# Performance work log

Hardware: AMD Instinct MI355X
Metric: run time of the kernel (lower is better)

## Reference

```python
import jax, jax.numpy as jnp
import numpy as np

B, T, S = 8, 96, 192          # batch, tgt_len (decoder steps), src_len (encoder memory)
D_IN, D_MEM = 512, 512        # input_size (query dim), mem_size (memory dim)


def setup_inputs() -> dict:
    key = jax.random.key(0)
    ks = jax.random.split(key, 9)
    w = 0.02  # init scale for learned params
    inputs = jax.random.normal(ks[0], (B, T, D_IN), jnp.float32)
    mems = jax.random.normal(ks[1], (B, S, D_MEM), jnp.float32)
    # lengths in [1, S] so no row is fully masked
    mem_masks = jax.random.randint(ks[2], (B,), 1, S + 1)
    Wq = jax.random.normal(ks[3], (D_MEM, D_IN), jnp.float32) * w    # linear_q.weight (no bias)
    Wc = jax.random.normal(ks[4], (D_MEM, D_MEM), jnp.float32) * w   # linear_c.weight
    bc = jax.random.normal(ks[5], (D_MEM,), jnp.float32) * w         # linear_c.bias
    v = jax.random.normal(ks[6], (D_MEM,), jnp.float32) * w          # v.weight (mem_size -> 1)
    Wout = jax.random.normal(ks[7], (D_IN, D_MEM + D_IN), jnp.float32) * w  # linear_out.weight
    bout = jax.random.normal(ks[8], (D_IN,), jnp.float32) * w        # linear_out.bias
    return dict(inputs=inputs, mems=mems, mem_masks=mem_masks,
                Wq=Wq, Wc=Wc, bc=bc, v=v, Wout=Wout, bout=bout)


def reference(inputs, mems, mem_masks, Wq, Wc, bc, v, Wout, bout):
    # score(): additive (tanh-MLP) attention
    wq = jnp.einsum('btd,md->btm', inputs, Wq)          # [B,T,Dm]
    uh = jnp.einsum('bsd,md->bsm', mems, Wc) + bc        # [B,S,Dm]
    # broadcast-add -> tanh -> project with v : [B,T,S]
    align = jnp.einsum('btsm,m->bts', jnp.tanh(wq[:, :, None, :] + uh[:, None, :, :]), v)
    # sequence_mask from lengths, applied along src dim
    mask = jnp.arange(S) < mem_masks[:, None]            # [B,S] bool
    align = jnp.where(mask[:, None, :], align, -jnp.inf)
    align_vectors = jax.nn.softmax(align, axis=-1)       # [B,T,S]
    c = jnp.einsum('bts,bsd->btd', align_vectors, mems)  # context [B,T,Dm]
    attn_h = jnp.concatenate([c, inputs], axis=-1) @ Wout.T + bout  # [B,T,D_IN]
    return attn_h, align_vectors
```

## Files before the change

### kernel.cpp

```cpp
#include <hip/hip_runtime.h>
#include <math.h>

#define BB 8
#define TT 96
#define SS 192
#define DIN 512
#define DM 512

typedef short short8 __attribute__((ext_vector_type(8)));
typedef float f32x4 __attribute__((ext_vector_type(4)));

__device__ __forceinline__ unsigned short f2bf(float f) {
    unsigned int u = __float_as_uint(f);
    unsigned int r = u + 0x7FFFu + ((u >> 16) & 1u);
    return (unsigned short)(r >> 16);
}
__device__ __forceinline__ float bf2f(unsigned short h) {
    return __uint_as_float(((unsigned int)h) << 16);
}

__device__ __forceinline__ void load_lds16(const void* g, void* l) {
    __builtin_amdgcn_global_load_lds((__attribute__((address_space(1))) void*)g,
                                     (__attribute__((address_space(3))) void*)l,
                                     16, 0, 0);
}

__global__ __launch_bounds__(256) void prep_cvt(
    const float* __restrict__ s0, const float* __restrict__ s1,
    const float* __restrict__ s2, const float* __restrict__ s3,
    const float* __restrict__ s4,
    unsigned short* __restrict__ d0, unsigned short* __restrict__ d1,
    unsigned short* __restrict__ d2, unsigned short* __restrict__ d3,
    unsigned short* __restrict__ d4)
{
    int bid = blockIdx.x;
    const float* s; unsigned short* d; int base;
    if (bid < 192)      { s = s0; d = d0; base = bid * 2048; }
    else if (bid < 576) { s = s1; d = d1; base = (bid - 192) * 2048; }
    else if (bid < 704) { s = s2; d = d2; base = (bid - 576) * 2048; }
    else if (bid < 832) { s = s3; d = d3; base = (bid - 704) * 2048; }
    else                { s = s4; d = d4; base = (bid - 832) * 2048; }
    int idx = base + threadIdx.x * 8;
    float4 a = *(const float4*)(s + idx);
    float4 b = *(const float4*)(s + idx + 4);
    short8 o;
    o[0] = (short)f2bf(a.x); o[1] = (short)f2bf(a.y);
    o[2] = (short)f2bf(a.z); o[3] = (short)f2bf(a.w);
    o[4] = (short)f2bf(b.x); o[5] = (short)f2bf(b.y);
    o[6] = (short)f2bf(b.z); o[7] = (short)f2bf(b.w);
    *(short8*)(d + idx) = o;
}

__device__ __forceinline__ void gemm_tile(
    unsigned short* As, unsigned short* Ws,
    const unsigned short* __restrict__ A, int lda,
    const unsigned short* __restrict__ W, int ldw,
    const float* __restrict__ bias,
    float* __restrict__ outF, unsigned short* __restrict__ outB,
    int bm, int bn, int N, int K)
{
    const int tid = threadIdx.x;
    const int r  = tid >> 2;
    const int kc = (tid & 3) * 8;
    const int lane = tid & 63, wv = tid >> 6;
    const int quad = lane >> 4, mrow = lane & 15;

    f32x4 acc0 = {0,0,0,0}, acc1 = {0,0,0,0}, acc2 = {0,0,0,0}, acc3 = {0,0,0,0};

    const unsigned short* arow = A + (size_t)(bm + r) * lda;
    const unsigned short* wrow = W + (size_t)(bn + r) * ldw;

    load_lds16(arow + kc,      As + tid * 8);
    load_lds16(wrow + kc,      Ws + tid * 8);
    load_lds16(arow + 32 + kc, As + 2048 + tid * 8);
    load_lds16(wrow + 32 + kc, Ws + 2048 + tid * 8);

    const int NC = K >> 5;
    int cur = 0;
    for (int c = 0; c < NC; ++c) {
        if (c + 2 < NC) {
            int nb = cur + 2; if (nb >= 3) nb -= 3;
            int gk = ((c + 2) << 5) + kc;
            load_lds16(arow + gk, As + nb * 2048 + tid * 8);
            load_lds16(wrow + gk, Ws + nb * 2048 + tid * 8);
            asm volatile("s_waitcnt vmcnt(4)" ::: "memory");
        } else if (c + 1 < NC) {
            asm volatile("s_waitcnt vmcnt(2)" ::: "memory");
        } else {
            asm volatile("s_waitcnt vmcnt(0)" ::: "memory");
        }
        __builtin_amdgcn_s_barrier();
        __builtin_amdgcn_sched_barrier(0);
        const unsigned short* Ab = As + cur * 2048;
        const unsigned short* Wb = Ws + cur * 2048;
        short8 av = *(const short8*)(Ab + (wv * 16 + mrow) * 32 + quad * 8);
        short8 b0 = *(const short8*)(Wb + (mrow) * 32 + quad * 8);
        short8 b1 = *(const short8*)(Wb + (16 + mrow) * 32 + quad * 8);
        short8 b2 = *(const short8*)(Wb + (32 + mrow) * 32 + quad * 8);
        short8 b3 = *(const short8*)(Wb + (48 + mrow) * 32 + quad * 8);
        acc0 = __builtin_amdgcn_mfma_f32_16x16x32_bf16(av, b0, acc0, 0, 0, 0);
        acc1 = __builtin_amdgcn_mfma_f32_16x16x32_bf16(av, b1, acc1, 0, 0, 0);
        acc2 = __builtin_amdgcn_mfma_f32_16x16x32_bf16(av, b2, acc2, 0, 0, 0);
        acc3 = __builtin_amdgcn_mfma_f32_16x16x32_bf16(av, b3, acc3, 0, 0, 0);
        __builtin_amdgcn_sched_barrier(0);
        __builtin_amdgcn_s_barrier();
        cur += 1; if (cur >= 3) cur -= 3;
    }

    f32x4 accs[4] = {acc0, acc1, acc2, acc3};
    #pragma unroll
    for (int ct = 0; ct < 4; ++ct) {
        int col = bn + ct * 16 + mrow;
        float bv = bias ? bias[col] : 0.0f;
        #pragma unroll
        for (int rg = 0; rg < 4; ++rg) {
            int rw = bm + wv * 16 + quad * 4 + rg;
            float val = accs[ct][rg] + bv;
            if (outF) outF[(size_t)rw * N + col] = val;
            else      outB[(size_t)rw * N + col] = f2bf(val);
        }
    }
}

__global__ __launch_bounds__(256) void proj_gemm(
    const unsigned short* __restrict__ inputs_bf,
    const unsigned short* __restrict__ mems_bf,
    const unsigned short* __restrict__ Wq_bf,
    const unsigned short* __restrict__ Wc_bf,
    const float* __restrict__ bc,
    const unsigned short* __restrict__ Wout_bf,
    const float* __restrict__ bout,
    unsigned short* __restrict__ wq_o, unsigned short* __restrict__ uh_o,
    unsigned short* __restrict__ m2_o, float* __restrict__ ih_o)
{
    __shared__ __align__(16) unsigned short As[3 * 2048];
    __shared__ __align__(16) unsigned short Ws[3 * 2048];
    int bid = blockIdx.x;
    if (bid < 96) {
        gemm_tile(As, Ws, inputs_bf, DIN, Wq_bf, DIN, nullptr, nullptr, wq_o,
                  (bid >> 3) * 64, (bid & 7) * 64, DM, DIN);
    } else if (bid < 288) {
        bid -= 96;
        gemm_tile(As, Ws, mems_bf, DM, Wc_bf, DM, bc, nullptr, uh_o,
                  (bid >> 3) * 64, (bid & 7) * 64, DM, DM);
    } else if (bid < 480) {
        bid -= 288;
        gemm_tile(As, Ws, mems_bf, DM, Wout_bf, DM + DIN, nullptr, nullptr, m2_o,
                  (bid >> 3) * 64, (bid & 7) * 64, DM, DM);
    } else {
        bid -= 480;
        gemm_tile(As, Ws, inputs_bf, DIN, Wout_bf + DM, DM + DIN, bout, ih_o, nullptr,
                  (bid >> 3) * 64, (bid & 7) * 64, DIN, DIN);
    }
}

__global__ __launch_bounds__(256) void attn_core(
    const unsigned short* __restrict__ wq,
    const unsigned short* __restrict__ uh,
    const float* __restrict__ v,
    const unsigned short* __restrict__ m2,
    const float* __restrict__ ih,
    const int* __restrict__ masks,
    float* __restrict__ align_out,
    float* __restrict__ attn_h)
{
    __shared__ float s_align[SS];
    __shared__ __align__(16) float s_part[4][DM];
    __shared__ float s_stat;
    const int row = blockIdx.x, b = row / TT;
    const int tid = threadIdx.x, lane = tid & 63, wid = tid >> 6;
    const int len = masks[b];
    const float C = 2.885390082f;

    if (tid >= len && tid < SS) s_align[tid] = -INFINITY;

    float cqf[8], vf[8];
    {
        short8 q = *(const short8*)(wq + (size_t)row * DM + lane * 8);
        float4 v0 = *(const float4*)(v + lane * 8);
        float4 v1 = *(const float4*)(v + lane * 8 + 4);
        #pragma unroll
        for (int j = 0; j < 8; ++j) cqf[j] = bf2f((unsigned short)q[j]) * C;
        vf[0] = v0.x; vf[1] = v0.y; vf[2] = v0.z; vf[3] = v0.w;
        vf[4] = v1.x; vf[5] = v1.y; vf[6] = v1.z; vf[7] = v1.w;
    }
    float SV = ((vf[0] + vf[1]) + (vf[2] + vf[3])) +
               ((vf[4] + vf[5]) + (vf[6] + vf[7]));
    #pragma unroll
    for (int off = 32; off; off >>= 1) SV += __shfl_xor(SV, off);

    #pragma unroll 2
    for (int s = wid; s < len; s += 4) {
        short8 u = *(const short8*)(uh + ((size_t)b * SS + s) * DM + lane * 8);
        float pr = 0.f;
        #pragma unroll
        for (int j = 0; j < 8; ++j) {
            float e = __builtin_amdgcn_exp2f(
                fmaf(bf2f((unsigned short)u[j]), C, cqf[j]));
            float rc = __builtin_amdgcn_rcpf(e + 1.f);
            pr = fmaf(vf[j], rc, pr);
        }
        #pragma unroll
        for (int off = 32; off; off >>= 1)
            pr += __shfl_xor(pr, off);
        if (lane == 0) s_align[s] = fmaf(-2.f, pr, SV);
    }
    __syncthreads();

    if (tid < 64) {
        float m = fmaxf(fmaxf(s_align[tid], s_align[tid + 64]), s_align[tid + 128]);
        #pragma unroll
        for (int off = 32; off; off >>= 1) m = fmaxf(m, __shfl_xor(m, off));
        float e0 = __builtin_amdgcn_exp2f((s_align[tid]       - m) * 1.44269504f);
        float e1 = __builtin_amdgcn_exp2f((s_align[tid + 64]  - m) * 1.44269504f);
        float e2 = __builtin_amdgcn_exp2f((s_align[tid + 128] - m) * 1.44269504f);
        s_align[tid] = e0; s_align[tid + 64] = e1; s_align[tid + 128] = e2;
        float sum = e0 + e1 + e2;
        #pragma unroll
        for (int off = 32; off; off >>= 1) sum += __shfl_xor(sum, off);
        if (tid == 0) s_stat = 1.0f / sum;
    }
    __syncthreads();
    const float inv = s_stat;
    if (tid < SS) align_out[(size_t)row * SS + tid] = s_align[tid] * inv;

    const int sbase = wid * 48;
    int nloc = len - sbase;
    nloc = nloc < 0 ? 0 : (nloc > 48 ? 48 : nloc);
    float accv[8] = {0,0,0,0,0,0,0,0};
    const unsigned short* m2b = m2 + ((size_t)b * SS + sbase) * DM + lane * 8;
    #pragma unroll 4
    for (int i = 0; i < nloc; ++i) {
        float p = s_align[sbase + i];
        short8 mv = *(const short8*)(m2b + (size_t)i * DM);
        #pragma unroll
        for (int j = 0; j < 8; ++j)
            accv[j] = fmaf(p, bf2f((unsigned short)mv[j]), accv[j]);
    }
    {
        float4 t0; t0.x = accv[0]; t0.y = accv[1]; t0.z = accv[2]; t0.w = accv[3];
        float4 t1; t1.x = accv[4]; t1.y = accv[5]; t1.z = accv[6]; t1.w = accv[7];
        *(float4*)&s_part[wid][lane * 8]     = t0;
        *(float4*)&s_part[wid][lane * 8 + 4] = t1;
    }
    __syncthreads();

    const int d0 = tid * 2;
    float r0 = s_part[0][d0]     + s_part[1][d0]     + s_part[2][d0]     + s_part[3][d0];
    float r1 = s_part[0][d0 + 1] + s_part[1][d0 + 1] + s_part[2][d0 + 1] + s_part[3][d0 + 1];
    float2 ihv = *(const float2*)(ih + (size_t)row * DIN + d0);
    float2 o;
    o.x = fmaf(r0, inv, ihv.x);
    o.y = fmaf(r1, inv, ihv.y);
    *(float2*)(attn_h + (size_t)row * DIN + d0) = o;
}

extern "C" void kernel_launch(void* const* d_in, const int* in_sizes, int n_in,
                              void* d_out, int out_size, void* d_ws, size_t ws_size,
                              hipStream_t stream) {
    (void)in_sizes; (void)n_in; (void)out_size; (void)ws_size;
    const float* inputs = (const float*)d_in[0];
    const float* mems   = (const float*)d_in[1];
    const int*   masks  = (const int*)  d_in[2];
    const float* Wq     = (const float*)d_in[3];
    const float* Wc     = (const float*)d_in[4];
    const float* bc     = (const float*)d_in[5];
    const float* v      = (const float*)d_in[6];
    const float* Wout   = (const float*)d_in[7];
    const float* bout   = (const float*)d_in[8];

    unsigned short* p = (unsigned short*)d_ws;
    unsigned short* inputs_bf = p;        p += 393216;
    unsigned short* mems_bf   = p;        p += 786432;
    unsigned short* Wq_bf     = p;        p += 262144;
    unsigned short* Wc_bf     = p;        p += 262144;
    unsigned short* Wout_bf   = p;        p += 524288;
    unsigned short* uh_bf     = p;        p += 786432;
    unsigned short* wq_bf     = p;        p += 393216;
    unsigned short* m2_bf     = p;        p += 786432;
    float* ih                 = (float*)p;

    float* attn_h    = (float*)d_out;
    float* align_out = attn_h + (size_t)BB * TT * DIN;

    prep_cvt<<<1088, 256, 0, stream>>>(inputs, mems, Wq, Wc, Wout,
                                       inputs_bf, mems_bf, Wq_bf, Wc_bf, Wout_bf);
    proj_gemm<<<576, 256, 0, stream>>>(inputs_bf, mems_bf, Wq_bf, Wc_bf, bc,
                                       Wout_bf, bout, wq_bf, uh_bf, m2_bf, ih);
    attn_core<<<BB * TT, 256, 0, stream>>>(wq_bf, uh_bf, v, m2_bf, ih, masks,
                                           align_out, attn_h);
}
```

Before: 115.2 us.

## Fuse prep, projection GEMMs and attention into one cooperative kernel

Merges the three kernel launches into one cooperative kernel of 768 blocks that runs the bf16 conversion, the projection GEMMs and the attention core in sequence, separated by grid-wide barriers. Shared memory is reused across phases through a single byte buffer. The goal is to remove inter-kernel launch gaps and tail drain. In exchange it adds grid.sync costs and fixes the grid size (768 blocks, launch bounds of 3 blocks per SM), leaving many blocks idle in the GEMM phase. It falls back to the original three launches if the cooperative launch fails.

```diff
diff --git a/kernel.cpp b/kernel.cpp
--- a/kernel.cpp
+++ b/kernel.cpp
@@ -1,5 +1,8 @@
 #include <hip/hip_runtime.h>
+#include <hip/hip_cooperative_groups.h>
 #include <math.h>
+
+namespace cg = cooperative_groups;
 
 #define BB 8
 #define TT 96
@@ -25,30 +28,29 @@
                                      16, 0, 0);
 }
 
-__global__ __launch_bounds__(256) void prep_cvt(
-    const float* __restrict__ s0, const float* __restrict__ s1,
-    const float* __restrict__ s2, const float* __restrict__ s3,
-    const float* __restrict__ s4,
-    unsigned short* __restrict__ d0, unsigned short* __restrict__ d1,
-    unsigned short* __restrict__ d2, unsigned short* __restrict__ d3,
-    unsigned short* __restrict__ d4)
-{
-    int bid = blockIdx.x;
-    const float* s; unsigned short* d; int base;
-    if (bid < 192)      { s = s0; d = d0; base = bid * 2048; }
-    else if (bid < 576) { s = s1; d = d1; base = (bid - 192) * 2048; }
-    else if (bid < 704) { s = s2; d = d2; base = (bid - 576) * 2048; }
-    else if (bid < 832) { s = s3; d = d3; base = (bid - 704) * 2048; }
-    else                { s = s4; d = d4; base = (bid - 832) * 2048; }
-    int idx = base + threadIdx.x * 8;
-    float4 a = *(const float4*)(s + idx);
-    float4 b = *(const float4*)(s + idx + 4);
+__device__ __forceinline__ void prep_one(
+    int idx,
+    const float* __restrict__ inputs, const float* __restrict__ mems,
+    const float* __restrict__ Wq, const float* __restrict__ Wc,
+    const float* __restrict__ Wout,
+    unsigned short* __restrict__ inputs_bf, unsigned short* __restrict__ mems_bf,
+    unsigned short* __restrict__ Wq_bf, unsigned short* __restrict__ Wc_bf,
+    unsigned short* __restrict__ Wout_bf)
+{
+    const float* s; unsigned short* d; int off;
+    if (idx < 393216)       { s = inputs; d = inputs_bf; off = idx; }
+    else if (idx < 1179648) { s = mems;   d = mems_bf;   off = idx - 393216; }
+    else if (idx < 1441792) { s = Wq;     d = Wq_bf;     off = idx - 1179648; }
+    else if (idx < 1703936) { s = Wc;     d = Wc_bf;     off = idx - 1441792; }
+    else                    { s = Wout;   d = Wout_bf;   off = idx - 1703936; }
+    float4 a = *(const float4*)(s + off);
+    float4 b = *(const float4*)(s + off + 4);
     short8 o;
     o[0] = (short)f2bf(a.x); o[1] = (short)f2bf(a.y);
     o[2] = (short)f2bf(a.z); o[3] = (short)f2bf(a.w);
     o[4] = (short)f2bf(b.x); o[5] = (short)f2bf(b.y);
     o[6] = (short)f2bf(b.z); o[7] = (short)f2bf(b.w);
-    *(short8*)(d + idx) = o;
+    *(short8*)(d + off) = o;
 }
 
 __device__ __forceinline__ void gemm_tile(
@@ -122,7 +124,8 @@
     }
 }
 
-__global__ __launch_bounds__(256) void proj_gemm(
+__device__ __forceinline__ void proj_dispatch(
+    int bid, unsigned short* As, unsigned short* Ws,
     const unsigned short* __restrict__ inputs_bf,
     const unsigned short* __restrict__ mems_bf,
     const unsigned short* __restrict__ Wq_bf,
@@ -133,9 +136,6 @@
     unsigned short* __restrict__ wq_o, unsigned short* __restrict__ uh_o,
     unsigned short* __restrict__ m2_o, float* __restrict__ ih_o)
 {
-    __shared__ __align__(16) unsigned short As[3 * 2048];
-    __shared__ __align__(16) unsigned short Ws[3 * 2048];
-    int bid = blockIdx.x;
     if (bid < 96) {
         gemm_tile(As, Ws, inputs_bf, DIN, Wq_bf, DIN, nullptr, nullptr, wq_o,
                   (bid >> 3) * 64, (bid & 7) * 64, DM, DIN);
@@ -154,20 +154,14 @@
     }
 }
 
-__global__ __launch_bounds__(256) void attn_core(
-    const unsigned short* __restrict__ wq,
-    const unsigned short* __restrict__ uh,
-    const float* __restrict__ v,
-    const unsigned short* __restrict__ m2,
-    const float* __restrict__ ih,
-    const int* __restrict__ masks,
-    float* __restrict__ align_out,
-    float* __restrict__ attn_h)
-{
-    __shared__ float s_align[SS];
-    __shared__ __align__(16) float s_part[4][DM];
-    __shared__ float s_stat;
-    const int row = blockIdx.x, b = row / TT;
+__device__ __forceinline__ void attn_body(
+    int row, float* s_align, float (*s_part)[DM], float* s_stat_p,
+    const unsigned short* __restrict__ wq, const unsigned short* __restrict__ uh,
+    const float* __restrict__ v, const unsigned short* __restrict__ m2,
+    const float* __restrict__ ih, const int* __restrict__ masks,
+    float* __restrict__ align_out, float* __restrict__ attn_h)
+{
+    const int b = row / TT;
     const int tid = threadIdx.x, lane = tid & 63, wid = tid >> 6;
     const int len = masks[b];
     const float C = 2.885390082f;
@@ -218,10 +212,10 @@
         float sum = e0 + e1 + e2;
         #pragma unroll
         for (int off = 32; off; off >>= 1) sum += __shfl_xor(sum, off);
-        if (tid == 0) s_stat = 1.0f / sum;
+        if (tid == 0) s_stat_p[0] = 1.0f / sum;
     }
     __syncthreads();
-    const float inv = s_stat;
+    const float inv = s_stat_p[0];
     if (tid < SS) align_out[(size_t)row * SS + tid] = s_align[tid] * inv;
 
     const int sbase = wid * 48;
@@ -253,6 +247,89 @@
     o.x = fmaf(r0, inv, ihv.x);
     o.y = fmaf(r1, inv, ihv.y);
     *(float2*)(attn_h + (size_t)row * DIN + d0) = o;
+}
+
+__global__ __launch_bounds__(256, 3) void fused_all(
+    const float* __restrict__ inputs, const float* __restrict__ mems,
+    const int* __restrict__ masks,
+    const float* __restrict__ Wq, const float* __restrict__ Wc,
+    const float* __restrict__ bc, const float* __restrict__ v,
+    const float* __restrict__ Wout, const float* __restrict__ bout,
+    unsigned short* __restrict__ inputs_bf, unsigned short* __restrict__ mems_bf,
+    unsigned short* __restrict__ Wq_bf, unsigned short* __restrict__ Wc_bf,
+    unsigned short* __restrict__ Wout_bf,
+    unsigned short* __restrict__ wq_bf, unsigned short* __restrict__ uh_bf,
+    unsigned short* __restrict__ m2_bf, float* __restrict__ ih,
+    float* __restrict__ align_out, float* __restrict__ attn_h)
+{
+    __shared__ __align__(16) unsigned char smem[24576];
+    cg::grid_group grid = cg::this_grid();
+    const int bid = blockIdx.x, tid = threadIdx.x;
+
+    for (int u8 = bid * 256 + tid; u8 < 278528; u8 += 768 * 256)
+        prep_one(u8 * 8, inputs, mems, Wq, Wc, Wout,
+                 inputs_bf, mems_bf, Wq_bf, Wc_bf, Wout_bf);
+    grid.sync();
+
+    if (bid < 576) {
+        unsigned short* As = (unsigned short*)smem;
+        unsigned short* Ws = As + 3 * 2048;
+        proj_dispatch(bid, As, Ws, inputs_bf, mems_bf, Wq_bf, Wc_bf, bc,
+                      Wout_bf, bout, wq_bf, uh_bf, m2_bf, ih);
+    }
+    grid.sync();
+
+    {
+        float* s_align = (float*)smem;
+        float (*s_part)[DM] = (float(*)[DM])(smem + 1024);
+        float* s_stat_p = (float*)(smem + 1024 + 8192);
+        attn_body(bid, s_align, s_part, s_stat_p,
+                  wq_bf, uh_bf, v, m2_bf, ih, masks, align_out, attn_h);
+    }
+}
+
+__global__ __launch_bounds__(256) void prep_cvt(
+    const float* __restrict__ inputs, const float* __restrict__ mems,
+    const float* __restrict__ Wq, const float* __restrict__ Wc,
+    const float* __restrict__ Wout,
+    unsigned short* __restrict__ inputs_bf, unsigned short* __restrict__ mems_bf,
+    unsigned short* __restrict__ Wq_bf, unsigned short* __restrict__ Wc_bf,
+    unsigned short* __restrict__ Wout_bf)
+{
+    int u8 = blockIdx.x * 256 + threadIdx.x;
+    if (u8 < 278528)
+        prep_one(u8 * 8, inputs, mems, Wq, Wc, Wout,
+                 inputs_bf, mems_bf, Wq_bf, Wc_bf, Wout_bf);
+}
+
+__global__ __launch_bounds__(256) void proj_gemm(
+    const unsigned short* __restrict__ inputs_bf,
+    const unsigned short* __restrict__ mems_bf,
+    const unsigned short* __restrict__ Wq_bf,
+    const unsigned short* __restrict__ Wc_bf,
+    const float* __restrict__ bc,
+    const unsigned short* __restrict__ Wout_bf,
+    const float* __restrict__ bout,
+    unsigned short* __restrict__ wq_o, unsigned short* __restrict__ uh_o,
+    unsigned short* __restrict__ m2_o, float* __restrict__ ih_o)
+{
+    __shared__ __align__(16) unsigned short As[3 * 2048];
+    __shared__ __align__(16) unsigned short Ws[3 * 2048];
+    proj_dispatch(blockIdx.x, As, Ws, inputs_bf, mems_bf, Wq_bf, Wc_bf, bc,
+                  Wout_bf, bout, wq_o, uh_o, m2_o, ih_o);
+}
+
+__global__ __launch_bounds__(256) void attn_core(
+    const unsigned short* __restrict__ wq, const unsigned short* __restrict__ uh,
+    const float* __restrict__ v, const unsigned short* __restrict__ m2,
+    const float* __restrict__ ih, const int* __restrict__ masks,
+    float* __restrict__ align_out, float* __restrict__ attn_h)
+{
+    __shared__ float s_align[SS];
+    __shared__ __align__(16) float s_part[4][DM];
+    __shared__ float s_stat;
+    attn_body(blockIdx.x, s_align, s_part, &s_stat,
+              wq, uh, v, m2, ih, masks, align_out, attn_h);
 }
 
 extern "C" void kernel_launch(void* const* d_in, const int* in_sizes, int n_in,
@@ -283,10 +360,24 @@
     float* attn_h    = (float*)d_out;
     float* align_out = attn_h + (size_t)BB * TT * DIN;
 
-    prep_cvt<<<1088, 256, 0, stream>>>(inputs, mems, Wq, Wc, Wout,
-                                       inputs_bf, mems_bf, Wq_bf, Wc_bf, Wout_bf);
-    proj_gemm<<<576, 256, 0, stream>>>(inputs_bf, mems_bf, Wq_bf, Wc_bf, bc,
-                                       Wout_bf, bout, wq_bf, uh_bf, m2_bf, ih);
-    attn_core<<<BB * TT, 256, 0, stream>>>(wq_bf, uh_bf, v, m2_bf, ih, masks,
-                                           align_out, attn_h);
-}
+    void* args[] = {
+        (void*)&inputs, (void*)&mems, (void*)&masks,
+        (void*)&Wq, (void*)&Wc, (void*)&bc, (void*)&v,
+        (void*)&Wout, (void*)&bout,
+        (void*)&inputs_bf, (void*)&mems_bf, (void*)&Wq_bf, (void*)&Wc_bf,
+        (void*)&Wout_bf, (void*)&wq_bf, (void*)&uh_bf, (void*)&m2_bf,
+        (void*)&ih, (void*)&align_out, (void*)&attn_h };
+
+    hipError_t e = hipLaunchCooperativeKernel(
+        reinterpret_cast<void*>(fused_all), dim3(768), dim3(256),
+        args, 0u, stream);
+
+    if (e != hipSuccess) {
+        prep_cvt<<<1088, 256, 0, stream>>>(inputs, mems, Wq, Wc, Wout,
+                                           inputs_bf, mems_bf, Wq_bf, Wc_bf, Wout_bf);
+        proj_gemm<<<576, 256, 0, stream>>>(inputs_bf, mems_bf, Wq_bf, Wc_bf, bc,
+                                           Wout_bf, bout, wq_bf, uh_bf, m2_bf, ih);
+        attn_core<<<BB * TT, 256, 0, stream>>>(wq_bf, uh_bf, v, m2_bf, ih, masks,
+                                               align_out, attn_h);
+    }
+}
```

Result: slower. 317.7 us (+175.8%).
